# Kernel tuning notes

Hardware: AMD Instinct MI355X
Metric: run time of the kernel (lower is better)

## Reference

```python
import jax, jax.numpy as jnp
import numpy as np

B, D_IN, D_H = 4096, 1024, 2048


def setup_inputs() -> dict:
    key = jax.random.key(0)
    ks = jax.random.split(key, 16)
    s_in = 1.0 / np.sqrt(D_IN)
    s_h = 1.0 / np.sqrt(D_H)
    inp = {
        "x": jax.random.normal(ks[0], (B, D_IN), jnp.float32),
        "h_prev": jax.random.normal(ks[1], (B, D_H), jnp.float32),
        "c_prev": jax.random.normal(ks[2], (B, D_H), jnp.float32),
        "n_prev": jax.random.uniform(ks[3], (B, D_H), jnp.float32) + 0.5,
        # input-gate weights [D_H, D_IN] (torch Linear layout) + biases
        "Wz": jax.random.uniform(ks[4], (D_H, D_IN), jnp.float32, -s_in, s_in),
        "Wi": jax.random.uniform(ks[5], (D_H, D_IN), jnp.float32, -s_in, s_in),
        "Wf": jax.random.uniform(ks[6], (D_H, D_IN), jnp.float32, -s_in, s_in),
        "Wo": jax.random.uniform(ks[7], (D_H, D_IN), jnp.float32, -s_in, s_in),
        "bz": jax.random.uniform(ks[8], (D_H,), jnp.float32, -s_in, s_in),
        "bi": jax.random.uniform(ks[9], (D_H,), jnp.float32, -s_in, s_in),
        "bf": jax.random.uniform(ks[10], (D_H,), jnp.float32, -s_in, s_in),
        "bo": jax.random.uniform(ks[11], (D_H,), jnp.float32, -s_in, s_in),
        # recurrent weights [D_H, D_H], bias-free
        "Rz": jax.random.uniform(ks[12], (D_H, D_H), jnp.float32, -s_h, s_h),
        "Ri": jax.random.uniform(ks[13], (D_H, D_H), jnp.float32, -s_h, s_h),
        "Rf": jax.random.uniform(ks[14], (D_H, D_H), jnp.float32, -s_h, s_h),
        "Ro": jax.random.uniform(ks[15], (D_H, D_H), jnp.float32, -s_h, s_h),
    }
    return inp


def reference(x, h_prev, c_prev, n_prev,
              Wz, Wi, Wf, Wo, bz, bi, bf, bo,
              Rz, Ri, Rf, Ro):
    # Fuse the 4 input GEMMs and 4 recurrent GEMMs into two batched contractions.
    Wcat = jnp.concatenate([Wz, Wi, Wf, Wo], axis=0)      # [4H, D_IN]
    Rcat = jnp.concatenate([Rz, Ri, Rf, Ro], axis=0)      # [4H, H]
    bcat = jnp.concatenate([bz, bi, bf, bo], axis=0)      # [4H]
    pre = x @ Wcat.T + h_prev @ Rcat.T + bcat              # [B, 4H]
    az, ai, af, ao = jnp.split(pre, 4, axis=1)
    z = jnp.tanh(az)
    i = jnp.exp(ai)
    f = jnp.exp(af)
    o = jax.nn.sigmoid(ao)
    c = f * c_prev + i * z
    n = f * n_prev + i
    h = o * (c / n)
    return h
```

## Files before the change

### kernel.cpp

```cpp
#include <hip/hip_runtime.h>
#include <hip/hip_fp16.h>

#define B_SZ  4096
#define DIN   1024
#define DH    2048
#define K_TOT 3072
#define N_TOT 8192

#define BM 256
#define BN 256
#define BK 64
#define NK (K_TOT / BK)

typedef _Float16 half8 __attribute__((ext_vector_type(8)));
typedef float   float4v __attribute__((ext_vector_type(4)));

__device__ __forceinline__ void load_lds16(const void* g, void* l) {
    __builtin_amdgcn_global_load_lds(
        (const __attribute__((address_space(1))) void*)g,
        (__attribute__((address_space(3))) void*)l,
        16, 0, 0);
}

#define A_BLOCKS ((B_SZ * K_TOT / 8) / 256)
#define W_BLOCKS ((N_TOT * K_TOT / 8) / 256)

__global__ __launch_bounds__(256) void cast_all_kernel(
        const float* __restrict__ x, const float* __restrict__ h,
        const float* __restrict__ Wz, const float* __restrict__ Wi,
        const float* __restrict__ Wf, const float* __restrict__ Wo,
        const float* __restrict__ Rz, const float* __restrict__ Ri,
        const float* __restrict__ Rf, const float* __restrict__ Ro,
        _Float16* __restrict__ A, _Float16* __restrict__ Wb) {
    const float* src;
    _Float16* dst;
    if (blockIdx.x < A_BLOCKS) {
        int idx = (blockIdx.x * 256 + threadIdx.x) * 8;
        int b = idx / K_TOT;
        int c = idx - b * K_TOT;
        src = (c < DIN) ? (x + (size_t)b * DIN + c) : (h + (size_t)b * DH + (c - DIN));
        dst = A + idx;
    } else {
        int idx = ((blockIdx.x - A_BLOCKS) * 256 + threadIdx.x) * 8;
        int n = idx / K_TOT;
        int c = idx - n * K_TOT;
        int g = (n >> 6) & 3;
        int j = ((n >> 8) << 6) | (n & 63);
        const float* W = (g == 0) ? Wz : (g == 1) ? Wi : (g == 2) ? Wf : Wo;
        const float* R = (g == 0) ? Rz : (g == 1) ? Ri : (g == 2) ? Rf : Ro;
        src = (c < DIN) ? (W + (size_t)j * DIN + c) : (R + (size_t)j * DH + (c - DIN));
        dst = Wb + idx;
    }
    float4 v0 = *reinterpret_cast<const float4*>(src);
    float4 v1 = *reinterpret_cast<const float4*>(src + 4);
    half8 o;
    o[0] = (_Float16)v0.x; o[1] = (_Float16)v0.y;
    o[2] = (_Float16)v0.z; o[3] = (_Float16)v0.w;
    o[4] = (_Float16)v1.x; o[5] = (_Float16)v1.y;
    o[6] = (_Float16)v1.z; o[7] = (_Float16)v1.w;
    *reinterpret_cast<half8*>(dst) = o;
}

__global__ __launch_bounds__(512, 2) void slstm_gemm_kernel(
        const _Float16* __restrict__ A, const _Float16* __restrict__ Wb,
        const float* __restrict__ c_prev, const float* __restrict__ n_prev,
        const float* __restrict__ bz, const float* __restrict__ bi,
        const float* __restrict__ bf, const float* __restrict__ bo,
        float* __restrict__ Hout) {
    __shared__ __align__(16) _Float16 As[2][BM * BK];
    __shared__ __align__(16) _Float16 Bs[2][BN * BK];

    const int bid   = blockIdx.x;
    const int swz   = (bid & 7) * 64 + (bid >> 3);
    const int ntile = swz & 31;
    const int mtile = swz >> 5;
    const int m0 = mtile * BM;
    const int n0 = ntile * BN;

    const int tid  = threadIdx.x;
    const int wv   = tid >> 6;
    const int wm   = wv >> 2;
    const int wn   = wv & 3;
    const int l    = tid & 63;
    const int quad = l >> 4;
    const int l16  = l & 15;

    float4v acc[8][4];
#pragma unroll
    for (int i = 0; i < 8; i++)
#pragma unroll
        for (int j = 0; j < 4; j++) acc[i][j] = (float4v){0.f, 0.f, 0.f, 0.f};

    const int lrow  = l >> 3;
    const int skoff = ((l & 7) ^ lrow) * 8;
    const _Float16* Ag = A  + (size_t)(m0 + wv * 16 + lrow) * K_TOT + skoff;
    const _Float16* Bg = Wb + (size_t)(n0 + wv * 16 + lrow) * K_TOT + skoff;
    const int ldsA = wv * 1024;

#define STAGE_A(h, nb, kk) do { \
    load_lds16(Ag + (size_t)(h) * 128 * K_TOT + (kk),        &As[nb][(h) * 8192 + ldsA]); \
    load_lds16(Ag + ((size_t)(h) * 128 + 8) * K_TOT + (kk),  &As[nb][(h) * 8192 + ldsA + 512]); } while (0)
#define STAGE_B(h, nb, kk) do { \
    load_lds16(Bg + (size_t)(h) * 128 * K_TOT + (kk),        &Bs[nb][(h) * 8192 + ldsA]); \
    load_lds16(Bg + ((size_t)(h) * 128 + 8) * K_TOT + (kk),  &Bs[nb][(h) * 8192 + ldsA + 512]); } while (0)

    const int aRowBase = wm * 16 + l16;
    const int bColBase = wn * 16 + l16;
    const int sl0 = ((0 + quad) ^ (l16 & 7)) * 8;
    const int sl1 = ((4 + quad) ^ (l16 & 7)) * 8;

    half8 afr[4][2], bfr0[2][2], bfr1[2][2];

#define LOAD_A(MB) \
    _Pragma("unroll") \
    for (int mf = 0; mf < 4; ++mf) { \
        const _Float16* p = Ac + (size_t)(aRowBase + ((MB) + mf) * 32) * BK; \
        afr[mf][0] = *reinterpret_cast<const half8*>(p + sl0); \
        afr[mf][1] = *reinterpret_cast<const half8*>(p + sl1); \
    }
#define LOAD_B(DST, NB) \
    _Pragma("unroll") \
    for (int nf = 0; nf < 2; ++nf) { \
        const _Float16* p = Bc + (size_t)(bColBase + ((NB) + nf) * 64) * BK; \
        DST[nf][0] = *reinterpret_cast<const half8*>(p + sl0); \
        DST[nf][1] = *reinterpret_cast<const half8*>(p + sl1); \
    }
#define MFMA16(MB, NB, BF) \
    _Pragma("unroll") \
    for (int kp = 0; kp < 2; ++kp) \
    _Pragma("unroll") \
    for (int mf = 0; mf < 4; ++mf) \
    _Pragma("unroll") \
    for (int nf = 0; nf < 2; ++nf) \
        acc[(MB) + mf][(NB) + nf] = __builtin_amdgcn_mfma_f32_16x16x32_f16( \
            afr[mf][kp], BF[nf][kp], acc[(MB) + mf][(NB) + nf], 0, 0, 0);

    STAGE_A(0, 0, 0);
    STAGE_B(0, 0, 0);
    STAGE_B(1, 0, 0);
    STAGE_A(1, 0, 0);

    for (int kt = 0; kt < NK; ++kt) {
        const int cur = kt & 1;
        const int nxt = cur ^ 1;
        const int kk  = (kt + 1 < NK) ? (kt + 1) * BK : 0;
        const _Float16* Ac = &As[cur][0];
        const _Float16* Bc = &Bs[cur][0];

        asm volatile("s_waitcnt vmcnt(4)" ::: "memory");
        __builtin_amdgcn_s_barrier();
        LOAD_A(0);
        LOAD_B(bfr0, 0);
        STAGE_A(0, nxt, kk);
        __builtin_amdgcn_s_setprio(1);
        MFMA16(0, 0, bfr0);
        __builtin_amdgcn_s_setprio(0);

        asm volatile("s_waitcnt vmcnt(4)" ::: "memory");
        __builtin_amdgcn_s_barrier();
        LOAD_B(bfr1, 2);
        STAGE_B(0, nxt, kk);
        __builtin_amdgcn_s_setprio(1);
        MFMA16(0, 2, bfr1);
        __builtin_amdgcn_s_setprio(0);

        asm volatile("s_waitcnt vmcnt(4)" ::: "memory");
        __builtin_amdgcn_s_barrier();
        LOAD_A(4);
        STAGE_B(1, nxt, kk);
        __builtin_amdgcn_s_setprio(1);
        MFMA16(4, 2, bfr1);
        __builtin_amdgcn_s_setprio(0);

        __builtin_amdgcn_s_barrier();
        STAGE_A(1, nxt, kk);
        __builtin_amdgcn_s_setprio(1);
        MFMA16(4, 0, bfr0);
        __builtin_amdgcn_s_setprio(0);
    }

    const int j = ntile * 64 + wn * 16 + l16;
    const float bzv = bz[j], biv = bi[j], bfv = bf[j], bov = bo[j];
#pragma unroll
    for (int mf = 0; mf < 8; ++mf) {
#pragma unroll
        for (int r = 0; r < 4; ++r) {
            const int row = m0 + mf * 32 + wm * 16 + quad * 4 + r;
            const size_t off = (size_t)row * DH + j;
            const float az  = acc[mf][0][r] + bzv;
            const float ai  = acc[mf][1][r] + biv;
            const float af_ = acc[mf][2][r] + bfv;
            const float ao  = acc[mf][3][r] + bov;
            const float ax = fabsf(az);
            const float e2 = __expf(-2.0f * ax);
            float tz = __fdividef(1.0f - e2, 1.0f + e2);
            tz = (az >= 0.0f) ? tz : -tz;
            const float iv = __expf(ai);
            const float fv = __expf(af_);
            const float ov = __fdividef(1.0f, 1.0f + __expf(-ao));
            const float cc = fv * c_prev[off] + iv * tz;
            const float nn = fv * n_prev[off] + iv;
            Hout[off] = ov * __fdividef(cc, nn);
        }
    }
#undef STAGE_A
#undef STAGE_B
#undef LOAD_A
#undef LOAD_B
#undef MFMA16
}

extern "C" void kernel_launch(void* const* d_in, const int* in_sizes, int n_in,
                              void* d_out, int out_size, void* d_ws, size_t ws_size,
                              hipStream_t stream) {
    const float* x      = (const float*)d_in[0];
    const float* h_prev = (const float*)d_in[1];
    const float* c_prev = (const float*)d_in[2];
    const float* n_prev = (const float*)d_in[3];
    const float* Wz = (const float*)d_in[4];
    const float* Wi = (const float*)d_in[5];
    const float* Wf = (const float*)d_in[6];
    const float* Wo = (const float*)d_in[7];
    const float* bz = (const float*)d_in[8];
    const float* bi = (const float*)d_in[9];
    const float* bf = (const float*)d_in[10];
    const float* bo = (const float*)d_in[11];
    const float* Rz = (const float*)d_in[12];
    const float* Ri = (const float*)d_in[13];
    const float* Rf = (const float*)d_in[14];
    const float* Ro = (const float*)d_in[15];

    _Float16* A  = (_Float16*)d_ws;
    _Float16* Wb = A + (size_t)B_SZ * K_TOT;

    cast_all_kernel<<<A_BLOCKS + W_BLOCKS, 256, 0, stream>>>(
        x, h_prev, Wz, Wi, Wf, Wo, Rz, Ri, Rf, Ro, A, Wb);

    dim3 grid(N_TOT / BN * (B_SZ / BM));
    slstm_gemm_kernel<<<grid, 512, 0, stream>>>(
        A, Wb, c_prev, n_prev, bz, bi, bf, bo, (float*)d_out);
}
```

Measured before the change: 441.1 us.

## Restructure GEMM main loop into HipKittens-style 8-wave ping-pong schedule with split LDS halves

Splits the A and B shared-memory tiles into separate lo/hi half buffers and unrolls the K loop by two, so each 128-row quarter-tile is staged independently. Global-to-LDS loads for later K steps are issued earlier, and each MFMA cluster is bracketed by barriers and lgkmcnt waits. The aim is finer-grained overlap between memory traffic and matrix math. In exchange it adds many more barriers, and the waitcnt accounting is hand-tuned, which risks races or stalls.

```diff
diff --git a/kernel.cpp b/kernel.cpp
--- a/kernel.cpp
+++ b/kernel.cpp
@@ -67,8 +67,10 @@
         const float* __restrict__ bz, const float* __restrict__ bi,
         const float* __restrict__ bf, const float* __restrict__ bo,
         float* __restrict__ Hout) {
-    __shared__ __align__(16) _Float16 As[2][BM * BK];
-    __shared__ __align__(16) _Float16 Bs[2][BN * BK];
+    __shared__ __align__(16) _Float16 As0lo[128 * BK], As0hi[128 * BK];
+    __shared__ __align__(16) _Float16 As1lo[128 * BK], As1hi[128 * BK];
+    __shared__ __align__(16) _Float16 Bs0lo[128 * BK], Bs0hi[128 * BK];
+    __shared__ __align__(16) _Float16 Bs1lo[128 * BK], Bs1hi[128 * BK];
 
     const int bid   = blockIdx.x;
     const int swz   = (bid & 7) * 64 + (bid >> 3);
@@ -93,16 +95,15 @@
 
     const int lrow  = l >> 3;
     const int skoff = ((l & 7) ^ lrow) * 8;
-    const _Float16* Ag = A  + (size_t)(m0 + wv * 16 + lrow) * K_TOT + skoff;
-    const _Float16* Bg = Wb + (size_t)(n0 + wv * 16 + lrow) * K_TOT + skoff;
+    const _Float16* Ag0 = A  + (size_t)(m0 + wv * 16 + lrow) * K_TOT + skoff;
+    const _Float16* Ag1 = A  + (size_t)(m0 + 128 + wv * 16 + lrow) * K_TOT + skoff;
+    const _Float16* Bg0 = Wb + (size_t)(n0 + wv * 16 + lrow) * K_TOT + skoff;
+    const _Float16* Bg1 = Wb + (size_t)(n0 + 128 + wv * 16 + lrow) * K_TOT + skoff;
     const int ldsA = wv * 1024;
 
-#define STAGE_A(h, nb, kk) do { \
-    load_lds16(Ag + (size_t)(h) * 128 * K_TOT + (kk),        &As[nb][(h) * 8192 + ldsA]); \
-    load_lds16(Ag + ((size_t)(h) * 128 + 8) * K_TOT + (kk),  &As[nb][(h) * 8192 + ldsA + 512]); } while (0)
-#define STAGE_B(h, nb, kk) do { \
-    load_lds16(Bg + (size_t)(h) * 128 * K_TOT + (kk),        &Bs[nb][(h) * 8192 + ldsA]); \
-    load_lds16(Bg + ((size_t)(h) * 128 + 8) * K_TOT + (kk),  &Bs[nb][(h) * 8192 + ldsA + 512]); } while (0)
+#define STAGE(ARR, G, kk) do { \
+    load_lds16((G) + (kk),                     &ARR[ldsA]); \
+    load_lds16((G) + (size_t)8 * K_TOT + (kk), &ARR[ldsA + 512]); } while (0)
 
     const int aRowBase = wm * 16 + l16;
     const int bColBase = wn * 16 + l16;
@@ -111,17 +112,17 @@
 
     half8 afr[4][2], bfr0[2][2], bfr1[2][2];
 
-#define LOAD_A(MB) \
+#define LOAD_A8(ARR) \
     _Pragma("unroll") \
     for (int mf = 0; mf < 4; ++mf) { \
-        const _Float16* p = Ac + (size_t)(aRowBase + ((MB) + mf) * 32) * BK; \
+        const _Float16* p = ARR + (size_t)(aRowBase + mf * 32) * BK; \
         afr[mf][0] = *reinterpret_cast<const half8*>(p + sl0); \
         afr[mf][1] = *reinterpret_cast<const half8*>(p + sl1); \
     }
-#define LOAD_B(DST, NB) \
+#define LOAD_B4(DST, ARR) \
     _Pragma("unroll") \
     for (int nf = 0; nf < 2; ++nf) { \
-        const _Float16* p = Bc + (size_t)(bColBase + ((NB) + nf) * 64) * BK; \
+        const _Float16* p = ARR + (size_t)(bColBase + nf * 64) * BK; \
         DST[nf][0] = *reinterpret_cast<const half8*>(p + sl0); \
         DST[nf][1] = *reinterpret_cast<const half8*>(p + sl1); \
     }
@@ -135,48 +136,92 @@
         acc[(MB) + mf][(NB) + nf] = __builtin_amdgcn_mfma_f32_16x16x32_f16( \
             afr[mf][kp], BF[nf][kp], acc[(MB) + mf][(NB) + nf], 0, 0, 0);
 
-    STAGE_A(0, 0, 0);
-    STAGE_B(0, 0, 0);
-    STAGE_B(1, 0, 0);
-    STAGE_A(1, 0, 0);
-
-    for (int kt = 0; kt < NK; ++kt) {
-        const int cur = kt & 1;
-        const int nxt = cur ^ 1;
-        const int kk  = (kt + 1 < NK) ? (kt + 1) * BK : 0;
-        const _Float16* Ac = &As[cur][0];
-        const _Float16* Bc = &Bs[cur][0];
-
-        asm volatile("s_waitcnt vmcnt(4)" ::: "memory");
-        __builtin_amdgcn_s_barrier();
-        LOAD_A(0);
-        LOAD_B(bfr0, 0);
-        STAGE_A(0, nxt, kk);
+#define BARRIER() __builtin_amdgcn_s_barrier()
+#define WAIT_LGKM0() asm volatile("s_waitcnt lgkmcnt(0)" ::: "memory")
+
+    STAGE(As0lo, Ag0, 0);
+    STAGE(Bs0lo, Bg0, 0);
+    STAGE(Bs0hi, Bg1, 0);
+    STAGE(As0hi, Ag1, 0);
+    asm volatile("s_waitcnt vmcnt(4)" ::: "memory");
+    STAGE(As1lo, Ag0, BK);
+    STAGE(Bs1lo, Bg0, BK);
+    STAGE(Bs1hi, Bg1, BK);
+    asm volatile("s_waitcnt vmcnt(6)" ::: "memory");
+    BARRIER();
+
+    for (int kt = 0; kt < NK; kt += 2) {
+        const int k1 = (kt + 1) * BK;
+        const int k2 = (kt + 2 < NK ? kt + 2 : 0) * BK;
+        const int k3 = (kt + 3 < NK ? kt + 3 : 0) * BK;
+
+        LOAD_A8(As0lo);
+        LOAD_B4(bfr0, Bs0lo);
+        STAGE(As1hi, Ag1, k1);
+        asm volatile("s_waitcnt lgkmcnt(8)" ::: "memory");
+        BARRIER();
+        WAIT_LGKM0();
         __builtin_amdgcn_s_setprio(1);
         MFMA16(0, 0, bfr0);
         __builtin_amdgcn_s_setprio(0);
-
-        asm volatile("s_waitcnt vmcnt(4)" ::: "memory");
-        __builtin_amdgcn_s_barrier();
-        LOAD_B(bfr1, 2);
-        STAGE_B(0, nxt, kk);
+        BARRIER();
+        LOAD_B4(bfr1, Bs0hi);
+        STAGE(As0lo, Ag0, k2);
+        BARRIER();
+        WAIT_LGKM0();
         __builtin_amdgcn_s_setprio(1);
         MFMA16(0, 2, bfr1);
         __builtin_amdgcn_s_setprio(0);
-
-        asm volatile("s_waitcnt vmcnt(4)" ::: "memory");
-        __builtin_amdgcn_s_barrier();
-        LOAD_A(4);
-        STAGE_B(1, nxt, kk);
+        BARRIER();
+        LOAD_A8(As0hi);
+        STAGE(Bs0lo, Bg0, k2);
+        BARRIER();
+        WAIT_LGKM0();
         __builtin_amdgcn_s_setprio(1);
         MFMA16(4, 2, bfr1);
         __builtin_amdgcn_s_setprio(0);
-
-        __builtin_amdgcn_s_barrier();
-        STAGE_A(1, nxt, kk);
+        BARRIER();
+        STAGE(Bs0hi, Bg1, k2);
+        asm volatile("s_waitcnt vmcnt(6)" ::: "memory");
+        BARRIER();
         __builtin_amdgcn_s_setprio(1);
         MFMA16(4, 0, bfr0);
         __builtin_amdgcn_s_setprio(0);
+        BARRIER();
+
+        LOAD_A8(As1lo);
+        LOAD_B4(bfr0, Bs1lo);
+        STAGE(As0hi, Ag1, k2);
+        asm volatile("s_waitcnt lgkmcnt(8)" ::: "memory");
+        BARRIER();
+        WAIT_LGKM0();
+        __builtin_amdgcn_s_setprio(1);
+        MFMA16(0, 0, bfr0);
+        __builtin_amdgcn_s_setprio(0);
+        BARRIER();
+        LOAD_B4(bfr1, Bs1hi);
+        STAGE(As1lo, Ag0, k3);
+        BARRIER();
+        WAIT_LGKM0();
+        __builtin_amdgcn_s_setprio(1);
+        MFMA16(0, 2, bfr1);
+        __builtin_amdgcn_s_setprio(0);
+        BARRIER();
+        LOAD_A8(As1hi);
+        STAGE(Bs1lo, Bg0, k3);
+        BARRIER();
+        WAIT_LGKM0();
+        __builtin_amdgcn_s_setprio(1);
+        MFMA16(4, 2, bfr1);
+        __builtin_amdgcn_s_setprio(0);
+        BARRIER();
+        STAGE(Bs1hi, Bg1, k3);
+        asm volatile("s_waitcnt vmcnt(6)" ::: "memory");
+        BARRIER();
+        __builtin_amdgcn_s_setprio(1);
+        MFMA16(4, 0, bfr0);
+        __builtin_amdgcn_s_setprio(0);
+        BARRIER();
     }
 
     const int j = ntile * 64 + wn * 16 + l16;
@@ -203,11 +248,12 @@
             Hout[off] = ov * __fdividef(cc, nn);
         }
     }
-#undef STAGE_A
-#undef STAGE_B
-#undef LOAD_A
-#undef LOAD_B
+#undef STAGE
+#undef LOAD_A8
+#undef LOAD_B4
 #undef MFMA16
+#undef BARRIER
+#undef WAIT_LGKM0
 }
 
 extern "C" void kernel_launch(void* const* d_in, const int* in_sizes, int n_in,
```

New measurement: 435.0 us. About the same (-1.4%).
